# Kernel tuning notes

Measured on AMD Instinct MI355X. Metric: run time of the kernel, lower is better.

## Reference

```python
import jax, jax.numpy as jnp
import numpy as np

B = 16          # batch (num decode sequences)
H = 16          # num heads (== num kv heads)
D = 128         # head dim
BLOCK = 16      # tokens per cache block
BPS = 128       # blocks per sequence
NB = B * BPS    # total cache blocks = 2048
S = BPS * BLOCK # max context len per seq = 2048
SCALE = 0.08838834764831845  # 1/sqrt(128)


def setup_inputs() -> dict:
    key = jax.random.key(0)
    ks = jax.random.split(key, 5)
    q = jax.random.normal(ks[0], (B, H, D), dtype=jnp.float32)
    k = jax.random.normal(ks[1], (B, H, D), dtype=jnp.float32)
    v = jax.random.normal(ks[2], (B, H, D), dtype=jnp.float32)
    k_cache = jax.random.normal(ks[3], (NB, BLOCK, H, D), dtype=jnp.float32)
    v_cache = jax.random.normal(ks[4], (NB, BLOCK, H, D), dtype=jnp.float32)
    # identity paged layout: seq i owns blocks [i*BPS, (i+1)*BPS)
    block_tables = jnp.arange(NB, dtype=jnp.int32).reshape(B, BPS)
    # new token goes into the last slot of each sequence's last block
    slot_mapping = (jnp.arange(B, dtype=jnp.int32) * BPS + (BPS - 1)) * BLOCK + (BLOCK - 1)
    context_lens = jnp.full((B,), S, dtype=jnp.int32)
    return {"q": q, "k": k, "v": v, "k_cache": k_cache, "v_cache": v_cache,
            "block_tables": block_tables, "slot_mapping": slot_mapping,
            "context_lens": context_lens}


def reference(q, k, v, k_cache, v_cache, block_tables, slot_mapping, context_lens):
    nb, block_size, h, d = k_cache.shape
    b = q.shape[0]
    # --- store_kvcache: scatter new K/V token into flat cache (all slots valid) ---
    flat_k = k_cache.reshape(nb * block_size, h, d).at[slot_mapping].set(k)
    flat_v = v_cache.reshape(nb * block_size, h, d).at[slot_mapping].set(v)
    kc = flat_k.reshape(nb, block_size, h, d)
    vc = flat_v.reshape(nb, block_size, h, d)
    # --- paged gather: [B, BPS, BLOCK, H, D] -> [B, S, H, D] ---
    k_seq = kc[block_tables].reshape(b, -1, h, d)
    v_seq = vc[block_tables].reshape(b, -1, h, d)
    s = k_seq.shape[1]
    # --- masked single-token attention (q_len = 1) ---
    scores = jnp.einsum('bhd,bshd->bhs', q, k_seq) * SCALE
    mask = jnp.arange(s, dtype=jnp.int32)[None, :] < context_lens[:, None]  # [B, S]
    scores = jnp.where(mask[:, None, :], scores, -jnp.inf)
    p = jax.nn.softmax(scores, axis=-1)
    o = jnp.einsum('bhs,bshd->bhd', p, v_seq)  # [B, H, D]
    return o
```

## Files before the change

### kernel.cpp

```cpp
#include <hip/hip_runtime.h>
#include <math.h>

#define BB   16
#define HH   16
#define DD   128
#define BLK  16
#define BPS  128
#define SS   2048
#define SCALE_F 0.08838834764831845f
#define FIXED_M 20.0f

#define SPLIT 8
#define CHUNK (SS / SPLIT)
#define NT1   256
#define NW1   4
#define TPW1  (CHUNK / NW1)

__global__ __launch_bounds__(NT1, 8)
void pd_partial(const float* __restrict__ q,
                const float* __restrict__ knew,
                const float* __restrict__ vnew,
                const float* __restrict__ kc,
                const float* __restrict__ vc,
                const int*   __restrict__ bt,
                const int*   __restrict__ smap_g,
                const int*   __restrict__ clen,
                float*       __restrict__ ml,
                float*       __restrict__ pacc)
{
    __shared__ int   rb[CHUNK];
    __shared__ float part[NW1][DD];
    __shared__ int   smap[BB];
    __shared__ float reds[NW1];

    const int bid  = blockIdx.x;
    const int c    = bid & (SPLIT - 1);
    const int bh   = bid >> 3;
    const int b    = bh >> 4;
    const int h    = bh & 15;
    const int t    = threadIdx.x;
    const int lane = t & 63;
    const int wave = t >> 6;
    const int len  = clen[b];
    const int sbase = c * CHUNK;

    if (t < BB) smap[t] = smap_g[t];
    __syncthreads();

    {
        int s    = sbase + t;
        int pb   = bt[b * BPS + (s >> 4)];
        int slot = pb * BLK + (s & 15);
        int enc  = (slot * HH + h) * DD;
        #pragma unroll
        for (int j = 0; j < BB; ++j)
            if (slot == smap[j]) enc = -(j + 1);
        rb[t] = enc;
    }
    __syncthreads();

    const int half = lane >> 5;
    const int d4   = lane & 31;
    const float4 q4 = *(const float4*)(q + bh * DD + d4 * 4);
    const int w0 = wave * TPW1;

    float  l   = 0.f;
    float4 acc = make_float4(0.f, 0.f, 0.f, 0.f);
    #pragma unroll 4
    for (int i = 0; i < TPW1 / 2; ++i) {
        int sl  = w0 + i * 2 + half;
        int s   = sbase + sl;
        int enc = rb[sl];
        const float* kp;
        const float* vp;
        if (enc >= 0) {
            kp = kc + enc + d4 * 4;
            vp = vc + enc + d4 * 4;
        } else {
            int j = -enc - 1;
            kp = knew + (j * HH + h) * DD + d4 * 4;
            vp = vnew + (j * HH + h) * DD + d4 * 4;
        }
        float4 kv = *(const float4*)kp;
        float4 vv = *(const float4*)vp;
        float dot = q4.x * kv.x + q4.y * kv.y + q4.z * kv.z + q4.w * kv.w;
        dot += __shfl_xor(dot, 1);
        dot += __shfl_xor(dot, 2);
        dot += __shfl_xor(dot, 4);
        dot += __shfl_xor(dot, 8);
        dot += __shfl_xor(dot, 16);
        float p = (s < len) ? expf(dot * SCALE_F - FIXED_M) : 0.f;
        l += p;
        acc.x += p * vv.x;
        acc.y += p * vv.y;
        acc.z += p * vv.z;
        acc.w += p * vv.w;
    }

    acc.x += __shfl_xor(acc.x, 32);
    acc.y += __shfl_xor(acc.y, 32);
    acc.z += __shfl_xor(acc.z, 32);
    acc.w += __shfl_xor(acc.w, 32);
    l     += __shfl_xor(l, 32);
    if (lane < 32) *(float4*)&part[wave][d4 * 4] = acc;
    if (lane == 0) reds[wave] = l;
    __syncthreads();

    if (t < DD) {
        float o = part[0][t] + part[1][t] + part[2][t] + part[3][t];
        pacc[bid * DD + t] = o;
    }
    if (t == 0)
        ml[bid] = reds[0] + reds[1] + reds[2] + reds[3];
}

__global__ __launch_bounds__(DD)
void pd_combine(const float* __restrict__ ml,
                const float* __restrict__ pacc,
                float*       __restrict__ out)
{
    const int bh = blockIdx.x;
    const int t  = threadIdx.x;

    float den = 0.f, o = 0.f;
    #pragma unroll
    for (int i = 0; i < SPLIT; ++i) {
        den += ml[bh * SPLIT + i];
        o   += pacc[(bh * SPLIT + i) * DD + t];
    }
    out[bh * DD + t] = o / den;
}

extern "C" void kernel_launch(void* const* d_in, const int* in_sizes, int n_in,
                              void* d_out, int out_size, void* d_ws, size_t ws_size,
                              hipStream_t stream)
{
    const float* q    = (const float*)d_in[0];
    const float* knew = (const float*)d_in[1];
    const float* vnew = (const float*)d_in[2];
    const float* kc   = (const float*)d_in[3];
    const float* vc   = (const float*)d_in[4];
    const int*   bt   = (const int*)d_in[5];
    const int*   smap = (const int*)d_in[6];
    const int*   clen = (const int*)d_in[7];
    float*       out  = (float*)d_out;

    float* ml   = (float*)d_ws;
    float* pacc = (float*)d_ws + BB * HH * SPLIT;

    pd_partial<<<dim3(BB * HH * SPLIT), dim3(NT1), 0, stream>>>(
        q, knew, vnew, kc, vc, bt, smap, clen, ml, pacc);
    pd_combine<<<dim3(BB * HH), dim3(DD), 0, stream>>>(ml, pacc, out);
}
```

Baseline: 100.8 us.

## Stream cache blocks directly and patch new-token slots with post-hoc corrections

The per-token slot indirection through shared memory is replaced by a loop over physical blocks, using one uniform block-table lookup per block and fixed strides for all sixteen tokens. Slots that the scatter would overwrite are recorded in shared memory. Afterwards their stale contribution is subtracted and the new token's contribution is added to both the accumulator and the denominator. The aim is to remove the per-token indirection and branch and make addresses wave-uniform and predictable. The cost is extra correction work and a cap of 64 corrections per block, beyond which results would be wrong. Subtracting the stale term can also lose precision.

```diff
diff --git a/kernel.cpp b/kernel.cpp
--- a/kernel.cpp
+++ b/kernel.cpp
@@ -14,7 +14,7 @@
 #define CHUNK (SS / SPLIT)
 #define NT1   256
 #define NW1   4
-#define TPW1  (CHUNK / NW1)
+#define MAXC  64
 
 __global__ __launch_bounds__(NT1, 8)
 void pd_partial(const float* __restrict__ q,
@@ -28,10 +28,13 @@
                 float*       __restrict__ ml,
                 float*       __restrict__ pacc)
 {
-    __shared__ int   rb[CHUNK];
     __shared__ float part[NW1][DD];
     __shared__ int   smap[BB];
     __shared__ float reds[NW1];
+    __shared__ int   nCorr;
+    __shared__ int   corrTok[MAXC];
+    __shared__ int   corrJ[MAXC];
+    __shared__ float corrPn[MAXC], corrPs[MAXC];
 
     const int bid  = blockIdx.x;
     const int c    = bid & (SPLIT - 1);
@@ -45,56 +48,55 @@
     const int sbase = c * CHUNK;
 
     if (t < BB) smap[t] = smap_g[t];
+    if (t == 0) nCorr = 0;
     __syncthreads();
 
     {
         int s    = sbase + t;
         int pb   = bt[b * BPS + (s >> 4)];
         int slot = pb * BLK + (s & 15);
-        int enc  = (slot * HH + h) * DD;
+        int match = -1;
         #pragma unroll
         for (int j = 0; j < BB; ++j)
-            if (slot == smap[j]) enc = -(j + 1);
-        rb[t] = enc;
+            if (slot == smap[j]) match = j;
+        if (match >= 0 && s < len) {
+            int idx = atomicAdd(&nCorr, 1);
+            if (idx < MAXC) { corrTok[idx] = t; corrJ[idx] = match; }
+        }
     }
-    __syncthreads();
 
     const int half = lane >> 5;
     const int d4   = lane & 31;
     const float4 q4 = *(const float4*)(q + bh * DD + d4 * 4);
-    const int w0 = wave * TPW1;
+    const int vOffEl = h * DD + half * (HH * DD) + d4 * 4;
 
     float  l   = 0.f;
     float4 acc = make_float4(0.f, 0.f, 0.f, 0.f);
-    #pragma unroll 4
-    for (int i = 0; i < TPW1 / 2; ++i) {
-        int sl  = w0 + i * 2 + half;
-        int s   = sbase + sl;
-        int enc = rb[sl];
-        const float* kp;
-        const float* vp;
-        if (enc >= 0) {
-            kp = kc + enc + d4 * 4;
-            vp = vc + enc + d4 * 4;
-        } else {
-            int j = -enc - 1;
-            kp = knew + (j * HH + h) * DD + d4 * 4;
-            vp = vnew + (j * HH + h) * DD + d4 * 4;
+    #pragma unroll
+    for (int g = 0; g < 4; ++g) {
+        int pbv = bt[b * BPS + c * 16 + wave * 4 + g];
+        int pb  = __builtin_amdgcn_readfirstlane(pbv);
+        const float* kbase = kc + (pb * (BLK * HH * DD) + vOffEl);
+        const float* vbase = vc + (pb * (BLK * HH * DD) + vOffEl);
+        const int sg = sbase + wave * 64 + g * 16;
+        #pragma unroll
+        for (int i2 = 0; i2 < 8; ++i2) {
+            float4 kv = *(const float4*)(kbase + i2 * 2 * (HH * DD));
+            float4 vv = *(const float4*)(vbase + i2 * 2 * (HH * DD));
+            float dot = q4.x * kv.x + q4.y * kv.y + q4.z * kv.z + q4.w * kv.w;
+            dot += __shfl_xor(dot, 1);
+            dot += __shfl_xor(dot, 2);
+            dot += __shfl_xor(dot, 4);
+            dot += __shfl_xor(dot, 8);
+            dot += __shfl_xor(dot, 16);
+            int s = sg + 2 * i2 + half;
+            float p = (s < len) ? __expf(dot * SCALE_F - FIXED_M) : 0.f;
+            l += p;
+            acc.x += p * vv.x;
+            acc.y += p * vv.y;
+            acc.z += p * vv.z;
+            acc.w += p * vv.w;
         }
-        float4 kv = *(const float4*)kp;
-        float4 vv = *(const float4*)vp;
-        float dot = q4.x * kv.x + q4.y * kv.y + q4.z * kv.z + q4.w * kv.w;
-        dot += __shfl_xor(dot, 1);
-        dot += __shfl_xor(dot, 2);
-        dot += __shfl_xor(dot, 4);
-        dot += __shfl_xor(dot, 8);
-        dot += __shfl_xor(dot, 16);
-        float p = (s < len) ? expf(dot * SCALE_F - FIXED_M) : 0.f;
-        l += p;
-        acc.x += p * vv.x;
-        acc.y += p * vv.y;
-        acc.z += p * vv.z;
-        acc.w += p * vv.w;
     }
 
     acc.x += __shfl_xor(acc.x, 32);
@@ -106,12 +108,49 @@
     if (lane == 0) reds[wave] = l;
     __syncthreads();
 
+    const int nC = (nCorr < MAXC) ? nCorr : MAXC;
+    if (wave == 0) {
+        for (int e = 0; e < nC; ++e) {
+            int tok = corrTok[e], j = corrJ[e];
+            int s    = sbase + tok;
+            int pb   = bt[b * BPS + (s >> 4)];
+            int slot = pb * BLK + (s & 15);
+            const float* krow = (lane < 32) ? (kc + (slot * HH + h) * DD)
+                                            : (knew + (j * HH + h) * DD);
+            float4 kq = *(const float4*)(krow + d4 * 4);
+            float dot = q4.x * kq.x + q4.y * kq.y + q4.z * kq.z + q4.w * kq.w;
+            dot += __shfl_xor(dot, 1);
+            dot += __shfl_xor(dot, 2);
+            dot += __shfl_xor(dot, 4);
+            dot += __shfl_xor(dot, 8);
+            dot += __shfl_xor(dot, 16);
+            float dS = __shfl(dot, 0);
+            float dN = __shfl(dot, 32);
+            if (lane == 0) {
+                corrPs[e] = __expf(dS * SCALE_F - FIXED_M);
+                corrPn[e] = __expf(dN * SCALE_F - FIXED_M);
+            }
+        }
+    }
+    __syncthreads();
+
     if (t < DD) {
         float o = part[0][t] + part[1][t] + part[2][t] + part[3][t];
+        for (int e = 0; e < nC; ++e) {
+            int tok = corrTok[e], j = corrJ[e];
+            int s    = sbase + tok;
+            int pb   = bt[b * BPS + (s >> 4)];
+            int slot = pb * BLK + (s & 15);
+            o += corrPn[e] * vnew[(j * HH + h) * DD + t]
+               - corrPs[e] * vc[(slot * HH + h) * DD + t];
+        }
         pacc[bid * DD + t] = o;
     }
-    if (t == 0)
-        ml[bid] = reds[0] + reds[1] + reds[2] + reds[3];
+    if (t == 0) {
+        float L = reds[0] + reds[1] + reds[2] + reds[3];
+        for (int e = 0; e < nC; ++e) L += corrPn[e] - corrPs[e];
+        ml[bid] = L;
+    }
 }
 
 __global__ __launch_bounds__(DD)
```

New measurement: 113.1 us. 12.3% more time.

## Process two adjacent heads per block for contiguous KV loads and double split

Applied to the files above, without the earlier changes.

Each block now handles two neighboring heads, with each half-wave computing one head, so a wave reads a contiguous 1KB span of K and V per token instead of 512B. The sequence split is doubled so the grid size stays the same, and expf is replaced by the fast __expf intrinsic. The intent is better memory coalescing on this bandwidth-bound decode attention. The cost is a larger workspace for partial results and more combine work per output.

```diff
diff --git a/kernel.cpp b/kernel.cpp
--- a/kernel.cpp
+++ b/kernel.cpp
@@ -3,6 +3,7 @@
 
 #define BB   16
 #define HH   16
+#define HP   (HH/2)
 #define DD   128
 #define BLK  16
 #define BPS  128
@@ -10,7 +11,7 @@
 #define SCALE_F 0.08838834764831845f
 #define FIXED_M 20.0f
 
-#define SPLIT 8
+#define SPLIT 16
 #define CHUNK (SS / SPLIT)
 #define NT1   256
 #define NW1   4
@@ -29,29 +30,32 @@
                 float*       __restrict__ pacc)
 {
     __shared__ int   rb[CHUNK];
-    __shared__ float part[NW1][DD];
+    __shared__ float part[NW1][2][DD];
     __shared__ int   smap[BB];
-    __shared__ float reds[NW1];
+    __shared__ float reds[NW1][2];
 
     const int bid  = blockIdx.x;
     const int c    = bid & (SPLIT - 1);
-    const int bh   = bid >> 3;
-    const int b    = bh >> 4;
-    const int h    = bh & 15;
+    const int bhp  = bid >> 4;
+    const int a    = bhp & (HP - 1);
+    const int b    = bhp >> 3;
+    const int h0   = 2 * a;
     const int t    = threadIdx.x;
     const int lane = t & 63;
     const int wave = t >> 6;
+    const int hh   = lane >> 5;
+    const int d4   = lane & 31;
     const int len  = clen[b];
     const int sbase = c * CHUNK;
 
     if (t < BB) smap[t] = smap_g[t];
     __syncthreads();
 
-    {
+    if (t < CHUNK) {
         int s    = sbase + t;
         int pb   = bt[b * BPS + (s >> 4)];
         int slot = pb * BLK + (s & 15);
-        int enc  = (slot * HH + h) * DD;
+        int enc  = (slot * HH + h0) * DD;
         #pragma unroll
         for (int j = 0; j < BB; ++j)
             if (slot == smap[j]) enc = -(j + 1);
@@ -59,27 +63,26 @@
     }
     __syncthreads();
 
-    const int half = lane >> 5;
-    const int d4   = lane & 31;
-    const float4 q4 = *(const float4*)(q + bh * DD + d4 * 4);
+    const float4 q4 = *(const float4*)(q + (b * HH + h0 + hh) * DD + d4 * 4);
     const int w0 = wave * TPW1;
+    const int lane4 = lane * 4;
 
     float  l   = 0.f;
     float4 acc = make_float4(0.f, 0.f, 0.f, 0.f);
     #pragma unroll 4
-    for (int i = 0; i < TPW1 / 2; ++i) {
-        int sl  = w0 + i * 2 + half;
+    for (int i = 0; i < TPW1; ++i) {
+        int sl  = w0 + i;
         int s   = sbase + sl;
         int enc = rb[sl];
         const float* kp;
         const float* vp;
         if (enc >= 0) {
-            kp = kc + enc + d4 * 4;
-            vp = vc + enc + d4 * 4;
+            kp = kc + enc + lane4;
+            vp = vc + enc + lane4;
         } else {
             int j = -enc - 1;
-            kp = knew + (j * HH + h) * DD + d4 * 4;
-            vp = vnew + (j * HH + h) * DD + d4 * 4;
+            kp = knew + (j * HH + h0) * DD + lane4;
+            vp = vnew + (j * HH + h0) * DD + lane4;
         }
         float4 kv = *(const float4*)kp;
         float4 vv = *(const float4*)vp;
@@ -89,7 +92,7 @@
         dot += __shfl_xor(dot, 4);
         dot += __shfl_xor(dot, 8);
         dot += __shfl_xor(dot, 16);
-        float p = (s < len) ? expf(dot * SCALE_F - FIXED_M) : 0.f;
+        float p = (s < len) ? __expf(dot * SCALE_F - FIXED_M) : 0.f;
         l += p;
         acc.x += p * vv.x;
         acc.y += p * vv.y;
@@ -97,21 +100,21 @@
         acc.w += p * vv.w;
     }
 
-    acc.x += __shfl_xor(acc.x, 32);
-    acc.y += __shfl_xor(acc.y, 32);
-    acc.z += __shfl_xor(acc.z, 32);
-    acc.w += __shfl_xor(acc.w, 32);
-    l     += __shfl_xor(l, 32);
-    if (lane < 32) *(float4*)&part[wave][d4 * 4] = acc;
-    if (lane == 0) reds[wave] = l;
+    *(float4*)&part[wave][hh][d4 * 4] = acc;
+    if (d4 == 0) reds[wave][hh] = l;
     __syncthreads();
 
-    if (t < DD) {
-        float o = part[0][t] + part[1][t] + part[2][t] + part[3][t];
-        pacc[bid * DD + t] = o;
+    {
+        int hidx = t >> 7;
+        int d    = t & 127;
+        int bh   = b * HH + h0 + hidx;
+        float o = part[0][hidx][d] + part[1][hidx][d]
+                + part[2][hidx][d] + part[3][hidx][d];
+        pacc[(bh * SPLIT + c) * DD + d] = o;
+        if (d == 0)
+            ml[bh * SPLIT + c] = reds[0][hidx] + reds[1][hidx]
+                               + reds[2][hidx] + reds[3][hidx];
     }
-    if (t == 0)
-        ml[bid] = reds[0] + reds[1] + reds[2] + reds[3];
 }
 
 __global__ __launch_bounds__(DD)
@@ -148,7 +151,7 @@
     float* ml   = (float*)d_ws;
     float* pacc = (float*)d_ws + BB * HH * SPLIT;
 
-    pd_partial<<<dim3(BB * HH * SPLIT), dim3(NT1), 0, stream>>>(
+    pd_partial<<<dim3(BB * HP * SPLIT), dim3(NT1), 0, stream>>>(
         q, knew, vnew, kc, vc, bt, smap, clen, ml, pacc);
     pd_combine<<<dim3(BB * HH), dim3(DD), 0, stream>>>(ml, pacc, out);
 }
```

Measured after the change: 105.7 us. 4.9% more time.
